# Kernel optimization log

Hardware: AMD Instinct MI355X
Metric: run time of the kernel (lower is better)

Reference implementation:

```python
import jax, jax.numpy as jnp
import numpy as np

VECT = 300   # word-vector dim
H = 128      # GRU hidden size
NSTACK = 3   # MultiHead stacks (shared SelfAttention weights)
SEQ = 4096


def _ln(x, g, b, eps=1e-5):
    m = jnp.mean(x, axis=-1, keepdims=True)
    v = jnp.mean((x - m) ** 2, axis=-1, keepdims=True)
    return g * (x - m) / jnp.sqrt(v + eps) + b


def _multihead(x, q_w, q_b, k_w, k_b, v_w, v_b, aln_g, aln_b, w_w, w_b, mln_g, mln_b):
    # x: [S, 300]. Same attention weights reused for all 3 stacks (as in source).
    scale = jnp.sqrt(jnp.asarray(float(VECT), x.dtype))
    out = x
    for _ in range(NSTACK):
        q = out @ q_w.T + q_b
        k = out @ k_w.T + k_b
        v = out @ v_w.T + v_b
        a = jax.nn.softmax((q @ k.T) / scale, axis=1)      # [S, S]
        h = _ln(a @ v + out, aln_g, aln_b)                  # SelfAttention out
        out = _ln(h @ w_w.T + w_b + x, mln_g, mln_b)        # residual to original x
    return out


def _gru(xs, w_ih, w_hh, b_ih, b_hh):
    # xs: [S, VECT]; PyTorch GRUCell math, h0 = zeros. Input projections batched.
    gx = xs @ w_ih.T + b_ih  # [S, 3H]
    def step(h, g):
        gh = h @ w_hh.T + b_hh
        r = jax.nn.sigmoid(g[:H] + gh[:H])
        z = jax.nn.sigmoid(g[H:2 * H] + gh[H:2 * H])
        n = jnp.tanh(g[2 * H:] + r * gh[2 * H:])
        return (1.0 - z) * n + z * h, None
    h, _ = jax.lax.scan(step, jnp.zeros((H,), xs.dtype), gx)
    return h


def setup_inputs() -> dict:
    key = jax.random.key(0)
    ks = jax.random.split(key, 16)

    def lin(k, o, i, s=0.05):
        k1, k2 = jax.random.split(k)
        return (jax.random.normal(k1, (o, i), jnp.float32) * s,
                jax.random.normal(k2, (o,), jnp.float32) * s)

    q_w, q_b = lin(ks[0], VECT, VECT)
    k_w, k_b = lin(ks[1], VECT, VECT)
    v_w, v_b = lin(ks[2], VECT, VECT)
    w_w, w_b = lin(ks[3], VECT, VECT)
    g1_wih, g1_bih = lin(ks[4], 3 * H, VECT)
    g1_whh, g1_bhh = lin(ks[5], 3 * H, H)
    g2_wih, g2_bih = lin(ks[6], 3 * H, VECT)
    g2_whh, g2_bhh = lin(ks[7], 3 * H, H)
    fc1_w, fc1_b = lin(ks[8], 256, 2 * H)
    fc2_w, fc2_b = lin(ks[9], 3, 256)

    return {
        'x1': jax.random.normal(ks[10], (SEQ, VECT), jnp.float32),
        'x2': jax.random.normal(ks[11], (SEQ, VECT), jnp.float32),
        'q_w': q_w, 'q_b': q_b, 'k_w': k_w, 'k_b': k_b, 'v_w': v_w, 'v_b': v_b,
        'aln_g': jnp.ones((VECT,), jnp.float32), 'aln_b': jnp.zeros((VECT,), jnp.float32),
        'w_w': w_w, 'w_b': w_b,
        'mln_g': jnp.ones((VECT,), jnp.float32), 'mln_b': jnp.zeros((VECT,), jnp.float32),
        'g1_wih': g1_wih, 'g1_whh': g1_whh, 'g1_bih': g1_bih, 'g1_bhh': g1_bhh,
        'g2_wih': g2_wih, 'g2_whh': g2_whh, 'g2_bih': g2_bih, 'g2_bhh': g2_bhh,
        'fc1_w': fc1_w, 'fc1_b': fc1_b, 'fc2_w': fc2_w, 'fc2_b': fc2_b,
    }


def reference(x1, x2, q_w, q_b, k_w, k_b, v_w, v_b, aln_g, aln_b, w_w, w_b,
              mln_g, mln_b, g1_wih, g1_whh, g1_bih, g1_bhh,
              g2_wih, g2_whh, g2_bih, g2_bhh, fc1_w, fc1_b, fc2_w, fc2_b):
    a1 = _multihead(x1, q_w, q_b, k_w, k_b, v_w, v_b, aln_g, aln_b, w_w, w_b, mln_g, mln_b)
    a2 = _multihead(x2, q_w, q_b, k_w, k_b, v_w, v_b, aln_g, aln_b, w_w, w_b, mln_g, mln_b)
    h1 = _gru(a1, g1_wih, g1_whh, g1_bih, g1_bhh)  # [H]
    h2 = _gru(a2, g2_wih, g2_whh, g2_bih, g2_bhh)  # [H]
    h = jnp.concatenate([h1, h2])[None, :]          # [1, 2H]
    h = jax.nn.relu(h @ fc1_w.T + fc1_b)
    return jax.nn.log_softmax(h @ fc2_w.T + fc2_b, axis=1)  # [1, 3]
```

## Files before the change

kernel.cpp:

```cpp
#include <hip/hip_runtime.h>
#include <hip/hip_bf16.h>

#define SEQL 4096
#define VECT 300
#define DP   320
#define NQT  20
#define HN   128
#define G3   384
#define JC   4
#define KROW 328
#define VROW 40
#define PROW 40

typedef unsigned short u16;
typedef unsigned char  u8;
typedef __attribute__((ext_vector_type(8))) short bf16x8;
typedef __attribute__((ext_vector_type(4))) float f32x4;
typedef __attribute__((ext_vector_type(4))) unsigned int u32x4;
typedef __attribute__((ext_vector_type(8))) int   v8i;

#define MFMA(a,b,c) __builtin_amdgcn_mfma_f32_16x16x32_bf16(a,b,c,0,0,0)

#define L2E 1.44269504088896f

#define RAW_BAR() do {                                          \
    asm volatile("s_waitcnt lgkmcnt(0)" ::: "memory");          \
    __builtin_amdgcn_s_barrier();                               \
    asm volatile("" ::: "memory");                              \
} while (0)

__device__ __forceinline__ float bf2f(u16 v){
    union { unsigned u; float f; } t; t.u = ((unsigned)v) << 16; return t.f;
}
__device__ __forceinline__ u16 f2bf(float f){
    union { float f; unsigned u; } t; t.f = f;
    return (u16)((t.u + 0x7FFFu + ((t.u >> 16) & 1u)) >> 16);
}
__device__ __forceinline__ float sigm_f(float x){
    return __builtin_amdgcn_rcpf(1.f + __builtin_amdgcn_exp2f(-L2E * x));
}
__device__ __forceinline__ float tanh_f(float x){
    return fmaf(2.f, __builtin_amdgcn_rcpf(1.f + __builtin_amdgcn_exp2f(-2.f * L2E * x)), -1.f);
}
__device__ __forceinline__ float sel4(f32x4 v, int r){
    float a = (r & 1) ? v.y : v.x;
    float b = (r & 1) ? v.w : v.z;
    return (r & 2) ? b : a;
}

__global__ __launch_bounds__(256) void pad_x2(const float* __restrict__ x1, const float* __restrict__ x2,
                                              float* __restrict__ xf, u16* __restrict__ cur)
{
    int s = blockIdx.y;
    const float* src = s ? x2 : x1;
    float* xfo = xf + (long)s * SEQL * DP;
    u16*  cro = cur + (long)s * SEQL * DP;
    int n = SEQL * DP;
    for (int i = blockIdx.x * blockDim.x + threadIdx.x; i < n; i += gridDim.x * blockDim.x){
        int r = i / DP, c = i - r * DP;
        float v = (c < VECT) ? src[r * VECT + c] : 0.f;
        xfo[i] = v;
        cro[i] = f2bf(v);
    }
}

__global__ __launch_bounds__(256) void cvt_pad_w4(const float* __restrict__ w0, const float* __restrict__ w1,
                                                  const float* __restrict__ w2, const float* __restrict__ w3,
                                                  u16* __restrict__ Wpk)
{
    int sl = blockIdx.y;
    const float* src = (sl == 0) ? w0 : (sl == 1) ? w1 : (sl == 2) ? w2 : w3;
    u16* dst = Wpk + (long)sl * DP * DP;
    int n = DP * DP;
    for (int i = blockIdx.x * blockDim.x + threadIdx.x; i < n; i += gridDim.x * blockDim.x){
        int r = i / DP, c = i - r * DP;
        float v = (r < VECT && c < VECT) ? src[r * VECT + c] : 0.f;
        dst[i] = f2bf(v);
    }
}

__global__ __launch_bounds__(256) void cvt_pad_g2(const float* __restrict__ w0, const float* __restrict__ w1,
                                                  u16* __restrict__ GWpk)
{
    int s = blockIdx.y;
    const float* src = s ? w1 : w0;
    u16* dst = GWpk + (long)s * G3 * DP;
    int n = G3 * DP;
    for (int i = blockIdx.x * blockDim.x + threadIdx.x; i < n; i += gridDim.x * blockDim.x){
        int r = i / DP, c = i - r * DP;
        float v = (c < VECT) ? src[r * VECT + c] : 0.f;
        dst[i] = f2bf(v);
    }
}

__global__ __launch_bounds__(256) void cvt_whh2(const float* __restrict__ w0, const float* __restrict__ w1,
                                                u8* __restrict__ dst0)
{
    int s = blockIdx.y;
    const float* src = s ? w1 : w0;
    u8* dst = dst0 + (long)s * G3 * HN;
    int idx = blockIdx.x * 256 + threadIdx.x;
    if (idx >= G3 * HN) return;
    int prow = idx >> 7, col = idx & 127;
    int w  = prow / 96, rem = prow - w * 96;
    int tg = rem / 48;  rem -= tg * 48;
    int g  = rem >> 4;  int rr = rem & 15;
    int orow = g * 128 + w * 32 + tg * 16 + rr;
    int pk = __builtin_amdgcn_cvt_pk_fp8_f32(src[orow * HN + col], 0.f, 0, false);
    dst[idx] = (u8)(pk & 0xFF);
}

template<int NT, int OM, bool WPERSEQ>
__global__ __launch_bounds__(256) void gemm_k(
    const u16* __restrict__ A, const u16* __restrict__ Wp,
    const float* __restrict__ b0, const float* __restrict__ b1, const float* __restrict__ b2,
    int nb, void* __restrict__ Out)
{
    const int lane = threadIdx.x & 63;
    const int wid  = threadIdx.x >> 6;
    const int s    = blockIdx.z;
    const int sl   = blockIdx.y;
    const int wsel = WPERSEQ ? s : sl;
    const int row0 = blockIdx.x * 64 + wid * 16;
    const int m    = lane & 15;
    const int q    = lane >> 4;

    const u16* Arow = A + ((long)s * SEQL + row0) * DP;
    const u16* W    = Wp + (long)wsel * (NT * 16) * DP;

    f32x4 zf = {0.f, 0.f, 0.f, 0.f};
    f32x4 acc[NT];
    #pragma unroll
    for (int n = 0; n < NT; n++) acc[n] = zf;

    for (int c = 0; c < DP / 32; ++c){
        const int koff = c * 32 + q * 8;
        bf16x8 a0 = *(const bf16x8*)(Arow + m * DP + koff);
        #pragma unroll
        for (int n = 0; n < NT; n++){
            bf16x8 b = *(const bf16x8*)(W + (n * 16 + m) * DP + koff);
            acc[n] = MFMA(a0, b, acc[n]);
        }
    }

    const int bsel = WPERSEQ ? s : sl;
    const float* bp = (bsel == 0) ? b0 : ((bsel == 1) ? b1 : b2);
    const long SLC = 2L * SEQL * DP;

    #pragma unroll
    for (int n = 0; n < NT; n++){
        int col = n * 16 + m;
        float bv = (col < nb) ? bp[col] : 0.f;
        #pragma unroll
        for (int r = 0; r < 4; r++){
            long row = row0 + q * 4 + r;
            float v = acc[n][r] + bv;
            if (OM == 4){
                int g = col >> 7, i2 = col & 127;
                long off = ((long)s * SEQL + row) * (long)(NT * 16) + (i2 * 3 + g);
                ((float*)Out)[off] = v;
            } else {
                long off;
                if (sl < 2) off = ((long)(sl * 2 + s) * SEQL + row) * DP + col;
                else        off = 2 * SLC + ((long)s * DP + col) * SEQL + row;
                ((u16*)Out)[off] = f2bf(v);
            }
        }
    }
}

__global__ __launch_bounds__(256) void gemmln_k(
    const u16* __restrict__ A, const u16* __restrict__ Wp, const float* __restrict__ bias,
    const float* __restrict__ res0, const float* __restrict__ res1,
    const float* __restrict__ g, const float* __restrict__ b,
    u16* __restrict__ OutB, float* __restrict__ OutF)
{
    const int lane = threadIdx.x & 63;
    const int wid  = threadIdx.x >> 6;
    const int s    = blockIdx.z;
    const int row0 = blockIdx.x * 64 + wid * 16;
    const int m    = lane & 15;
    const int q    = lane >> 4;

    const u16* Arow = A + ((long)s * SEQL + row0) * DP;
    const float* res = s ? res1 : res0;

    f32x4 zf = {0.f, 0.f, 0.f, 0.f};
    f32x4 acc[NQT];
    #pragma unroll
    for (int n = 0; n < NQT; n++) acc[n] = zf;

    for (int c = 0; c < DP / 32; ++c){
        const int koff = c * 32 + q * 8;
        bf16x8 a0 = *(const bf16x8*)(Arow + m * DP + koff);
        #pragma unroll
        for (int n = 0; n < NQT; n++){
            bf16x8 bb = *(const bf16x8*)(Wp + (n * 16 + m) * DP + koff);
            acc[n] = MFMA(a0, bb, acc[n]);
        }
    }

    float sum[4] = {0,0,0,0}, sq[4] = {0,0,0,0};
    #pragma unroll
    for (int n = 0; n < NQT; n++){
        int col = n * 16 + m;
        float bv = (col < VECT) ? bias[col] : 0.f;
        #pragma unroll
        for (int r = 0; r < 4; r++){
            long row = row0 + q * 4 + r;
            float rr = (col < VECT) ? res[row * VECT + col] : 0.f;
            float t = (col < VECT) ? (acc[n][r] + bv + rr) : 0.f;
            acc[n][r] = t;
            sum[r] += t; sq[r] += t * t;
        }
    }
    #pragma unroll
    for (int r = 0; r < 4; r++){
        float su = sum[r], sv = sq[r];
        su += __shfl_xor(su, 1); sv += __shfl_xor(sv, 1);
        su += __shfl_xor(su, 2); sv += __shfl_xor(sv, 2);
        su += __shfl_xor(su, 4); sv += __shfl_xor(sv, 4);
        su += __shfl_xor(su, 8); sv += __shfl_xor(sv, 8);
        sum[r] = su; sq[r] = sv;
    }
    float mean[4], rstd[4];
    #pragma unroll
    for (int r = 0; r < 4; r++){
        mean[r] = sum[r] / VECT;
        float var = sq[r] / VECT - mean[r] * mean[r];
        rstd[r] = rsqrtf(var + 1e-5f);
    }
    #pragma unroll
    for (int n = 0; n < NQT; n++){
        int col = n * 16 + m;
        float gv = (col < VECT) ? g[col] : 0.f;
        float bv = (col < VECT) ? b[col] : 0.f;
        #pragma unroll
        for (int r = 0; r < 4; r++){
            long row = (long)s * SEQL + row0 + q * 4 + r;
            float t = (col < VECT) ? ((acc[n][r] - mean[r]) * rstd[r] * gv + bv) : 0.f;
            OutB[row * DP + col] = f2bf(t);
            OutF[row * DP + col] = t;
        }
    }
}

__global__ __launch_bounds__(256, 1) void flash_k(
    const u16* __restrict__ Q, const u16* __restrict__ K, const u16* __restrict__ VT,
    u16* __restrict__ Onum, float* __restrict__ Lp)
{
    const int tid  = threadIdx.x;
    const int lane = tid & 63;
    const int wid  = tid >> 6;
    const int bid  = blockIdx.x;
    const int s    = bid & 1;
    const int jc   = (bid >> 1) & 3;
    const int xi   = bid >> 3;
    const int row0 = xi * 128 + wid * 32;
    const int m = lane & 15, q = lane >> 4;

    __shared__ __align__(16) u16 Kt[32 * KROW];
    __shared__ __align__(16) u16 Vt[DP * VROW];
    __shared__ __align__(16) u16 pb[4][2][16 * PROW];

    const u16* Qb = Q  + ((long)s * SEQL + row0) * DP;
    const u16* Kc = K  + (long)s * SEQL * DP + (long)jc * 1024 * DP;
    const u16* Vc = VT + (long)s * DP * SEQL + jc * 1024;

    bf16x8 qf0[10], qf1[10];
    #pragma unroll
    for (int c = 0; c < 10; c++){
        qf0[c] = *(const bf16x8*)(Qb + (m     ) * DP + c * 32 + q * 8);
        qf1[c] = *(const bf16x8*)(Qb + (m + 16) * DP + c * 32 + q * 8);
    }

    int skoff[5], wkoff[5], svoff[5], wvoff[5];
    #pragma unroll
    for (int it = 0; it < 5; it++){
        int f  = (it * 256 + tid) * 8;
        int rk = f / 320, ck = f - rk * 320;
        skoff[it] = f;
        wkoff[it] = rk * KROW + ck;
        int rv = f >> 5, cv = f & 31;
        svoff[it] = rv * SEQL + cv;
        wvoff[it] = rv * VROW + cv;
    }

    f32x4 zf = {0.f, 0.f, 0.f, 0.f};
    f32x4 oacc0[NQT], oacc1[NQT];
    #pragma unroll
    for (int n = 0; n < NQT; n++){ oacc0[n] = zf; oacc1[n] = zf; }
    float lacc0[4] = {0,0,0,0}, lacc1[4] = {0,0,0,0};

    const float K2 = 0.057735026918962576f * L2E;
    const float MB = -16.f * L2E;

    u32x4 kreg[5], vreg[5];
    #pragma unroll
    for (int it = 0; it < 5; it++){
        kreg[it] = *(const u32x4*)(Kc + skoff[it]);
        vreg[it] = *(const u32x4*)(Vc + svoff[it]);
    }
    #pragma unroll
    for (int it = 0; it < 5; it++){
        *(u32x4*)(&Kt[wkoff[it]]) = kreg[it];
        *(u32x4*)(&Vt[wvoff[it]]) = vreg[it];
    }
    RAW_BAR();

    u16* pb0 = &pb[wid][0][0];
    u16* pb1 = &pb[wid][1][0];

    for (int j = 0; j < 32; ++j){
        if (j + 1 < 32){
            const u16* Kj = Kc + (j + 1) * 32 * DP;
            const u16* Vj = Vc + (j + 1) * 32;
            #pragma unroll
            for (int it = 0; it < 5; it++){
                kreg[it] = *(const u32x4*)(Kj + skoff[it]);
                vreg[it] = *(const u32x4*)(Vj + svoff[it]);
            }
        }
        f32x4 s0A = zf, s0B = zf, s1A = zf, s1B = zf;
        #pragma unroll
        for (int c = 0; c < 10; c++){
            bf16x8 kA = *(const bf16x8*)(&Kt[(m     ) * KROW + c * 32 + q * 8]);
            bf16x8 kB = *(const bf16x8*)(&Kt[(m + 16) * KROW + c * 32 + q * 8]);
            s0A = MFMA(qf0[c], kA, s0A);
            s0B = MFMA(qf0[c], kB, s0B);
            s1A = MFMA(qf1[c], kA, s1A);
            s1B = MFMA(qf1[c], kB, s1B);
        }
        #pragma unroll
        for (int r = 0; r < 4; r++){
            float a0 = __builtin_amdgcn_exp2f(fmaf(s0A[r], K2, MB));
            float b0 = __builtin_amdgcn_exp2f(fmaf(s0B[r], K2, MB));
            float a1 = __builtin_amdgcn_exp2f(fmaf(s1A[r], K2, MB));
            float b1 = __builtin_amdgcn_exp2f(fmaf(s1B[r], K2, MB));
            lacc0[r] += a0 + b0;
            lacc1[r] += a1 + b1;
            pb0[(q * 4 + r) * PROW +      m] = f2bf(a0);
            pb0[(q * 4 + r) * PROW + 16 + m] = f2bf(b0);
            pb1[(q * 4 + r) * PROW +      m] = f2bf(a1);
            pb1[(q * 4 + r) * PROW + 16 + m] = f2bf(b1);
        }
        bf16x8 pf0 = *(const bf16x8*)(&pb0[m * PROW + q * 8]);
        bf16x8 pf1 = *(const bf16x8*)(&pb1[m * PROW + q * 8]);
        #pragma unroll
        for (int n = 0; n < NQT; n++){
            bf16x8 vb = *(const bf16x8*)(&Vt[(n * 16 + m) * VROW + q * 8]);
            oacc0[n] = MFMA(pf0, vb, oacc0[n]);
            oacc1[n] = MFMA(pf1, vb, oacc1[n]);
        }
        RAW_BAR();
        if (j + 1 < 32){
            #pragma unroll
            for (int it = 0; it < 5; it++){
                *(u32x4*)(&Kt[wkoff[it]]) = kreg[it];
                *(u32x4*)(&Vt[wvoff[it]]) = vreg[it];
            }
        }
        RAW_BAR();
    }

    #pragma unroll
    for (int r = 0; r < 4; r++){
        float t0 = lacc0[r], t1 = lacc1[r];
        t0 += __shfl_xor(t0, 1); t0 += __shfl_xor(t0, 2);
        t0 += __shfl_xor(t0, 4); t0 += __shfl_xor(t0, 8);
        t1 += __shfl_xor(t1, 1); t1 += __shfl_xor(t1, 2);
        t1 += __shfl_xor(t1, 4); t1 += __shfl_xor(t1, 8);
        lacc0[r] = t0; lacc1[r] = t1;
    }
    const long grow0 = (long)s * SEQL + row0;
    if (m == 0){
        #pragma unroll
        for (int r = 0; r < 4; r++){
            Lp[(long)jc * 2 * SEQL + grow0 +      q * 4 + r] = lacc0[r];
            Lp[(long)jc * 2 * SEQL + grow0 + 16 + q * 4 + r] = lacc1[r];
        }
    }
    u16* Ob = Onum + ((long)jc * 2 * SEQL + grow0) * DP;
    #pragma unroll
    for (int n = 0; n < NQT; n++)
        #pragma unroll
        for (int r = 0; r < 4; r++){
            Ob[(long)(     q * 4 + r) * DP + n * 16 + m] = f2bf(oacc0[n][r]);
            Ob[(long)(16 + q * 4 + r) * DP + n * 16 + m] = f2bf(oacc1[n][r]);
        }
}

__global__ __launch_bounds__(256) void lncomb_k(const u16* __restrict__ Onum, const float* __restrict__ Lp,
                                                const float* __restrict__ XF,
                                                const float* __restrict__ g, const float* __restrict__ b,
                                                u16* __restrict__ OutB)
{
    long row = (long)((blockIdx.x * blockDim.x + threadIdx.x) >> 6);
    int lane = threadIdx.x & 63;
    if (row >= 2L * SEQL) return;
    float l = 0.f;
    #pragma unroll
    for (int jc = 0; jc < JC; jc++) l += Lp[(long)jc * 2 * SEQL + row];
    float inv = 1.f / l;
    const float* xr = XF + row * DP;
    float v[5], sum = 0.f, sq = 0.f;
    #pragma unroll
    for (int i = 0; i < 5; i++){
        int c = lane + i * 64;
        float o = 0.f;
        #pragma unroll
        for (int jc = 0; jc < JC; jc++)
            o += bf2f(Onum[((long)jc * 2 * SEQL + row) * DP + c]);
        float t = (c < VECT) ? (o * inv + xr[c]) : 0.f;
        v[i] = t; sum += t; sq += t * t;
    }
    #pragma unroll
    for (int o = 1; o < 64; o <<= 1){ sum += __shfl_xor(sum, o); sq += __shfl_xor(sq, o); }
    float mean = sum / VECT;
    float var  = sq / VECT - mean * mean;
    float rstd = rsqrtf(var + 1e-5f);
    #pragma unroll
    for (int i = 0; i < 5; i++){
        int c = lane + i * 64;
        float t = (c < VECT) ? ((v[i] - mean) * rstd * g[c] + b[c]) : 0.f;
        OutB[row * DP + c] = f2bf(t);
    }
}

__global__ __launch_bounds__(256, 1) void gru_k(
    const float* __restrict__ GXP,
    const u8* __restrict__ Whh8p,
    const float* __restrict__ Bhh1, const float* __restrict__ Bhh2,
    float* __restrict__ Hout)
{
    const int s = blockIdx.x;
    const int tid = threadIdx.x;
    const int lane = tid & 63;
    const int wid  = tid >> 6;
    const int m = lane & 15, q = lane >> 4;
    const u8* Whh = Whh8p + (long)s * G3 * HN;
    const float* Bhh = s ? Bhh2 : Bhh1;
    const float* gx = GXP + (long)s * SEQL * G3;

    __shared__ __align__(8) u8 hst[2][HN];

    v8i af[6];
    #pragma unroll
    for (int tg = 0; tg < 2; tg++)
        #pragma unroll
        for (int g = 0; g < 3; g++)
            af[tg * 3 + g] = *(const v8i*)(Whh + (long)(wid * 96 + tg * 48 + g * 16 + m) * HN + q * 32);

    const int tgl  = (m >> 2) & 1;
    const int rsel = m & 3;
    const int il   = wid * 32 + tgl * 16 + q * 4 + rsel;
    const int il3  = il * 3;
    const float bhr = Bhh[il], bhz = Bhh[HN + il], bhn = Bhh[2 * HN + il];

    if (tid < HN){ hst[0][tid] = 0; hst[1][tid] = 0; }

    const float* ga = gx + il3;
    float cr0 = ga[0], cz0 = ga[1], cn0 = ga[2];
    const float* gb = gx + G3 + il3;
    float cr1 = gb[0], cz1 = gb[1], cn1 = gb[2];

    __syncthreads();

    float h = 0.f;
    const f32x4 zf = {0.f, 0.f, 0.f, 0.f};

#define GRU_STEP(T, CR, CZ, CN, WB, RB)                                               \
    {                                                                                 \
        v8i bfrag = *(const v8i*)(&hst[RB][q * 32]);                                  \
        f32x4 a0 = __builtin_amdgcn_mfma_scale_f32_16x16x128_f8f6f4(af[0], bfrag, zf, 0, 0, 0, 127, 0, 127); \
        f32x4 a1 = __builtin_amdgcn_mfma_scale_f32_16x16x128_f8f6f4(af[1], bfrag, zf, 0, 0, 0, 127, 0, 127); \
        f32x4 a2 = __builtin_amdgcn_mfma_scale_f32_16x16x128_f8f6f4(af[2], bfrag, zf, 0, 0, 0, 127, 0, 127); \
        f32x4 a3 = __builtin_amdgcn_mfma_scale_f32_16x16x128_f8f6f4(af[3], bfrag, zf, 0, 0, 0, 127, 0, 127); \
        f32x4 a4 = __builtin_amdgcn_mfma_scale_f32_16x16x128_f8f6f4(af[4], bfrag, zf, 0, 0, 0, 127, 0, 127); \
        f32x4 a5 = __builtin_amdgcn_mfma_scale_f32_16x16x128_f8f6f4(af[5], bfrag, zf, 0, 0, 0, 127, 0, 127); \
        float ghr = sel4(tgl ? a3 : a0, rsel);                                        \
        float ghz = sel4(tgl ? a4 : a1, rsel);                                        \
        float ghn = sel4(tgl ? a5 : a2, rsel);                                        \
        float rg = sigm_f(CR + ghr + bhr);                                            \
        float zg = sigm_f(CZ + ghz + bhz);                                            \
        float ng = tanh_f(CN + rg * (ghn + bhn));                                     \
        h = (1.f - zg) * ng + zg * h;                                                 \
        if (m < 8){                                                                   \
            int pk = __builtin_amdgcn_cvt_pk_fp8_f32(h, h, 0, false);                 \
            hst[WB][il] = (u8)(pk & 0xFF);                                            \
        }                                                                             \
        int tp = ((T) + 2 < SEQL) ? (T) + 2 : SEQL - 1;                               \
        const float* gp = gx + (long)tp * G3 + il3;                                   \
        CR = gp[0]; CZ = gp[1]; CN = gp[2];                                           \
        asm volatile("s_waitcnt lgkmcnt(0)" ::: "memory");                            \
        __builtin_amdgcn_s_barrier();                                                 \
        asm volatile("" ::: "memory");                                                \
    }

    for (int t = 0; t < SEQL; t += 2){
        GRU_STEP(t,     cr0, cz0, cn0, 0, 1);
        GRU_STEP(t + 1, cr1, cz1, cn1, 1, 0);
    }
#undef GRU_STEP

    if (m < 8) Hout[s * HN + il] = h;
}

__global__ __launch_bounds__(256) void final_k(const float* __restrict__ Hout,
                                               const float* __restrict__ fc1w, const float* __restrict__ fc1b,
                                               const float* __restrict__ fc2w, const float* __restrict__ fc2b,
                                               float* __restrict__ out)
{
    __shared__ float hb[256];
    __shared__ float r1[256];
    __shared__ float lg[3];
    int tid = threadIdx.x;
    hb[tid] = Hout[tid];
    __syncthreads();
    float a = 0.f;
    for (int k2 = 0; k2 < 256; k2++) a += hb[k2] * fc1w[tid * 256 + k2];
    a += fc1b[tid];
    r1[tid] = fmaxf(a, 0.f);
    __syncthreads();
    if (tid < 3){
        float v = 0.f;
        for (int k2 = 0; k2 < 256; k2++) v += r1[k2] * fc2w[tid * 256 + k2];
        lg[tid] = v + fc2b[tid];
    }
    __syncthreads();
    if (tid == 0){
        float mx = fmaxf(lg[0], fmaxf(lg[1], lg[2]));
        float se = __expf(lg[0] - mx) + __expf(lg[1] - mx) + __expf(lg[2] - mx);
        float ls = mx + logf(se);
        out[0] = lg[0] - ls;
        out[1] = lg[1] - ls;
        out[2] = lg[2] - ls;
    }
}

extern "C" void kernel_launch(void* const* d_in, const int* in_sizes, int n_in,
                              void* d_out, int out_size, void* d_ws, size_t ws_size,
                              hipStream_t stream)
{
    (void)in_sizes; (void)n_in; (void)out_size; (void)ws_size;
    const float* x1     = (const float*)d_in[0];
    const float* x2     = (const float*)d_in[1];
    const float* q_w    = (const float*)d_in[2],  *q_b   = (const float*)d_in[3];
    const float* k_w    = (const float*)d_in[4],  *k_b   = (const float*)d_in[5];
    const float* v_w    = (const float*)d_in[6],  *v_b   = (const float*)d_in[7];
    const float* aln_g  = (const float*)d_in[8],  *aln_b = (const float*)d_in[9];
    const float* w_w    = (const float*)d_in[10], *w_b   = (const float*)d_in[11];
    const float* mln_g  = (const float*)d_in[12], *mln_b = (const float*)d_in[13];
    const float* g1_wih = (const float*)d_in[14], *g1_whh = (const float*)d_in[15];
    const float* g1_bih = (const float*)d_in[16], *g1_bhh = (const float*)d_in[17];
    const float* g2_wih = (const float*)d_in[18], *g2_whh = (const float*)d_in[19];
    const float* g2_bih = (const float*)d_in[20], *g2_bhh = (const float*)d_in[21];
    const float* fc1w   = (const float*)d_in[22], *fc1b  = (const float*)d_in[23];
    const float* fc2w   = (const float*)d_in[24], *fc2b  = (const float*)d_in[25];

    char* wsp = (char*)d_ws;
    auto alloc = [&](size_t bytes) -> char* {
        char* p = wsp; wsp += (bytes + 255) & ~(size_t)255; return p;
    };
    float* XF   = (float*)alloc(2L * SEQL * DP * 4);
    u16*   CUR  = (u16*)  alloc(2L * SEQL * DP * 2);
    u16*   Hb   = (u16*)  alloc(2L * SEQL * DP * 2);
    u16*   Wpk  = (u16*)  alloc(4L * DP * DP * 2);
    u16*   GWpk = (u16*)  alloc(2L * G3 * DP * 2);
    u8*    Whh8 = (u8*)   alloc(2L * G3 * HN);
    float* Hout = (float*)alloc(2L * HN * 4);
    float* Lp   = (float*)alloc((long)JC * 2 * SEQL * 4);
    size_t u1 = (2L * 2 * SEQL * DP + 2L * DP * SEQL) * 2;
    size_t u1b = 2L * SEQL * G3 * 4;
    u16*   QKV  = (u16*)  alloc(u1 > u1b ? u1 : u1b);
    u16*   VT   = QKV + 2L * 2 * SEQL * DP;
    float* GX   = (float*)QKV;
    u16*   Onum = (u16*)  alloc((long)JC * 2 * SEQL * DP * 2);

    pad_x2<<<dim3(256, 2), 256, 0, stream>>>(x1, x2, XF, CUR);
    cvt_pad_w4<<<dim3(128, 4), 256, 0, stream>>>(q_w, k_w, v_w, w_w, Wpk);
    cvt_pad_g2<<<dim3(128, 2), 256, 0, stream>>>(g1_wih, g2_wih, GWpk);
    cvt_whh2<<<dim3(192, 2), 256, 0, stream>>>(g1_whh, g2_whh, Whh8);

    for (int st = 0; st < 3; ++st){
        gemm_k<NQT, 3, false><<<dim3(SEQL / 64, 3, 2), 256, 0, stream>>>(
            CUR, Wpk, q_b, k_b, v_b, VECT, QKV);
        flash_k<<<dim3(256), 256, 0, stream>>>(QKV, QKV + 2L*SEQL*DP, VT, Onum, Lp);
        lncomb_k<<<dim3(2 * SEQL / 4), 256, 0, stream>>>(Onum, Lp, XF, aln_g, aln_b, Hb);
        gemmln_k<<<dim3(SEQL / 64, 1, 2), 256, 0, stream>>>(
            Hb, Wpk + 3L * DP * DP, w_b, x1, x2, mln_g, mln_b, CUR, XF);
    }

    gemm_k<24, 4, true><<<dim3(SEQL / 64, 1, 2), 256, 0, stream>>>(
        CUR, GWpk, g1_bih, g2_bih, nullptr, G3, GX);
    gru_k<<<dim3(2), 256, 0, stream>>>(GX, Whh8, g1_bhh, g2_bhh, Hout);
    final_k<<<dim3(1), 256, 0, stream>>>(Hout, fc1w, fc1b, fc2w, fc2b, (float*)d_out);
}
```

Measured before the change: 2.026 ms.

## Halve per-wave query rows in flash kernel to double occupancy

Each wave in the attention kernel now handles 16 query rows instead of 32, so each block covers 64 rows and the grid doubles to 512 blocks. Launch bounds are raised to 2 blocks per CU. The aim is to cut register pressure from the accumulators and improve latency hiding and CU coverage. The cost is that each K/V tile loaded into shared memory is reused for half as many query rows, which doubles total K/V global traffic.

```diff
diff --git a/kernel.cpp b/kernel.cpp
--- a/kernel.cpp
+++ b/kernel.cpp
@@ -245,7 +245,7 @@
     }
 }
 
-__global__ __launch_bounds__(256, 1) void flash_k(
+__global__ __launch_bounds__(256, 2) void flash_k(
     const u16* __restrict__ Q, const u16* __restrict__ K, const u16* __restrict__ VT,
     u16* __restrict__ Onum, float* __restrict__ Lp)
 {
@@ -256,23 +256,21 @@
     const int s    = bid & 1;
     const int jc   = (bid >> 1) & 3;
     const int xi   = bid >> 3;
-    const int row0 = xi * 128 + wid * 32;
+    const int row0 = xi * 64 + wid * 16;
     const int m = lane & 15, q = lane >> 4;
 
     __shared__ __align__(16) u16 Kt[32 * KROW];
     __shared__ __align__(16) u16 Vt[DP * VROW];
-    __shared__ __align__(16) u16 pb[4][2][16 * PROW];
+    __shared__ __align__(16) u16 pb[4][16 * PROW];
 
     const u16* Qb = Q  + ((long)s * SEQL + row0) * DP;
     const u16* Kc = K  + (long)s * SEQL * DP + (long)jc * 1024 * DP;
     const u16* Vc = VT + (long)s * DP * SEQL + jc * 1024;
 
-    bf16x8 qf0[10], qf1[10];
-    #pragma unroll
-    for (int c = 0; c < 10; c++){
-        qf0[c] = *(const bf16x8*)(Qb + (m     ) * DP + c * 32 + q * 8);
-        qf1[c] = *(const bf16x8*)(Qb + (m + 16) * DP + c * 32 + q * 8);
-    }
+    bf16x8 qf[10];
+    #pragma unroll
+    for (int c = 0; c < 10; c++)
+        qf[c] = *(const bf16x8*)(Qb + m * DP + c * 32 + q * 8);
 
     int skoff[5], wkoff[5], svoff[5], wvoff[5];
     #pragma unroll
@@ -287,10 +285,10 @@
     }
 
     f32x4 zf = {0.f, 0.f, 0.f, 0.f};
-    f32x4 oacc0[NQT], oacc1[NQT];
-    #pragma unroll
-    for (int n = 0; n < NQT; n++){ oacc0[n] = zf; oacc1[n] = zf; }
-    float lacc0[4] = {0,0,0,0}, lacc1[4] = {0,0,0,0};
+    f32x4 oacc[NQT];
+    #pragma unroll
+    for (int n = 0; n < NQT; n++) oacc[n] = zf;
+    float lacc[4] = {0,0,0,0};
 
     const float K2 = 0.057735026918962576f * L2E;
     const float MB = -16.f * L2E;
@@ -308,8 +306,7 @@
     }
     RAW_BAR();
 
-    u16* pb0 = &pb[wid][0][0];
-    u16* pb1 = &pb[wid][1][0];
+    u16* pbw = &pb[wid][0];
 
     for (int j = 0; j < 32; ++j){
         if (j + 1 < 32){
@@ -321,36 +318,27 @@
                 vreg[it] = *(const u32x4*)(Vj + svoff[it]);
             }
         }
-        f32x4 s0A = zf, s0B = zf, s1A = zf, s1B = zf;
+        f32x4 sA = zf, sB = zf;
         #pragma unroll
         for (int c = 0; c < 10; c++){
             bf16x8 kA = *(const bf16x8*)(&Kt[(m     ) * KROW + c * 32 + q * 8]);
             bf16x8 kB = *(const bf16x8*)(&Kt[(m + 16) * KROW + c * 32 + q * 8]);
-            s0A = MFMA(qf0[c], kA, s0A);
-            s0B = MFMA(qf0[c], kB, s0B);
-            s1A = MFMA(qf1[c], kA, s1A);
-            s1B = MFMA(qf1[c], kB, s1B);
+            sA = MFMA(qf[c], kA, sA);
+            sB = MFMA(qf[c], kB, sB);
         }
         #pragma unroll
         for (int r = 0; r < 4; r++){
-            float a0 = __builtin_amdgcn_exp2f(fmaf(s0A[r], K2, MB));
-            float b0 = __builtin_amdgcn_exp2f(fmaf(s0B[r], K2, MB));
-            float a1 = __builtin_amdgcn_exp2f(fmaf(s1A[r], K2, MB));
-            float b1 = __builtin_amdgcn_exp2f(fmaf(s1B[r], K2, MB));
-            lacc0[r] += a0 + b0;
-            lacc1[r] += a1 + b1;
-            pb0[(q * 4 + r) * PROW +      m] = f2bf(a0);
-            pb0[(q * 4 + r) * PROW + 16 + m] = f2bf(b0);
-            pb1[(q * 4 + r) * PROW +      m] = f2bf(a1);
-            pb1[(q * 4 + r) * PROW + 16 + m] = f2bf(b1);
-        }
-        bf16x8 pf0 = *(const bf16x8*)(&pb0[m * PROW + q * 8]);
-        bf16x8 pf1 = *(const bf16x8*)(&pb1[m * PROW + q * 8]);
+            float a = __builtin_amdgcn_exp2f(fmaf(sA[r], K2, MB));
+            float b = __builtin_amdgcn_exp2f(fmaf(sB[r], K2, MB));
+            lacc[r] += a + b;
+            pbw[(q * 4 + r) * PROW +      m] = f2bf(a);
+            pbw[(q * 4 + r) * PROW + 16 + m] = f2bf(b);
+        }
+        bf16x8 pf = *(const bf16x8*)(&pbw[m * PROW + q * 8]);
         #pragma unroll
         for (int n = 0; n < NQT; n++){
             bf16x8 vb = *(const bf16x8*)(&Vt[(n * 16 + m) * VROW + q * 8]);
-            oacc0[n] = MFMA(pf0, vb, oacc0[n]);
-            oacc1[n] = MFMA(pf1, vb, oacc1[n]);
+            oacc[n] = MFMA(pf, vb, oacc[n]);
         }
         RAW_BAR();
         if (j + 1 < 32){
@@ -365,29 +353,23 @@
 
     #pragma unroll
     for (int r = 0; r < 4; r++){
-        float t0 = lacc0[r], t1 = lacc1[r];
+        float t0 = lacc[r];
         t0 += __shfl_xor(t0, 1); t0 += __shfl_xor(t0, 2);
         t0 += __shfl_xor(t0, 4); t0 += __shfl_xor(t0, 8);
-        t1 += __shfl_xor(t1, 1); t1 += __shfl_xor(t1, 2);
-        t1 += __shfl_xor(t1, 4); t1 += __shfl_xor(t1, 8);
-        lacc0[r] = t0; lacc1[r] = t1;
+        lacc[r] = t0;
     }
     const long grow0 = (long)s * SEQL + row0;
     if (m == 0){
         #pragma unroll
-        for (int r = 0; r < 4; r++){
-            Lp[(long)jc * 2 * SEQL + grow0 +      q * 4 + r] = lacc0[r];
-            Lp[(long)jc * 2 * SEQL + grow0 + 16 + q * 4 + r] = lacc1[r];
-        }
+        for (int r = 0; r < 4; r++)
+            Lp[(long)jc * 2 * SEQL + grow0 + q * 4 + r] = lacc[r];
     }
     u16* Ob = Onum + ((long)jc * 2 * SEQL + grow0) * DP;
     #pragma unroll
     for (int n = 0; n < NQT; n++)
         #pragma unroll
-        for (int r = 0; r < 4; r++){
-            Ob[(long)(     q * 4 + r) * DP + n * 16 + m] = f2bf(oacc0[n][r]);
-            Ob[(long)(16 + q * 4 + r) * DP + n * 16 + m] = f2bf(oacc1[n][r]);
-        }
+        for (int r = 0; r < 4; r++)
+            Ob[(long)(q * 4 + r) * DP + n * 16 + m] = f2bf(oacc[n][r]);
 }
 
 __global__ __launch_bounds__(256) void lncomb_k(const u16* __restrict__ Onum, const float* __restrict__ Lp,
@@ -585,7 +567,7 @@
     for (int st = 0; st < 3; ++st){
         gemm_k<NQT, 3, false><<<dim3(SEQL / 64, 3, 2), 256, 0, stream>>>(
             CUR, Wpk, q_b, k_b, v_b, VECT, QKV);
-        flash_k<<<dim3(256), 256, 0, stream>>>(QKV, QKV + 2L*SEQL*DP, VT, Onum, Lp);
+        flash_k<<<dim3(512), 256, 0, stream>>>(QKV, QKV + 2L*SEQL*DP, VT, Onum, Lp);
         lncomb_k<<<dim3(2 * SEQL / 4), 256, 0, stream>>>(Onum, Lp, XF, aln_g, aln_b, Hb);
         gemmln_k<<<dim3(SEQL / 64, 1, 2), 256, 0, stream>>>(
             Hb, Wpk + 3L * DP * DP, w_b, x1, x2, mln_g, mln_b, CUR, XF);
```

Result: no change. 2.004 ms (-1.1%).
